# Performance work log

Measured on AMD Instinct MI355X. Metric: run time of the kernel, lower is better.

## Reference

```python
import jax, jax.numpy as jnp
import numpy as np
from jax import lax

K = 4  # scan directions

def setup_inputs() -> dict:
    key = jax.random.key(0)
    ks = jax.random.split(key, 8)
    B, D, H, W = 8, 192, 64, 64
    N, R = 16, 6
    return {
        "x": jax.random.normal(ks[0], (B, D, H, W), jnp.float32),
        "x_proj_weight": jax.random.normal(ks[1], (K, R + 2 * N, D), jnp.float32) * (D ** -0.5),
        "dt_projs_weight": jax.random.normal(ks[2], (K, D, R), jnp.float32) * (R ** -0.5),
        "dt_projs_bias": jax.random.normal(ks[3], (K, D), jnp.float32) * 0.1,
        "A_logs": jax.random.uniform(ks[4], (K * D, N), jnp.float32, 0.0, 1.0),
        "Ds": jnp.ones((K * D,), jnp.float32),
        "out_norm_weight": jnp.ones((D,), jnp.float32),
        "out_norm_bias": jnp.zeros((D,), jnp.float32),
    }


def _ss2d_core(x, x_proj_weight, dt_projs_weight, dt_projs_bias, A_logs, Ds,
               out_norm_weight, out_norm_bias):
    B, D, H, W = x.shape
    L = H * W
    N = A_logs.shape[1]
    R = dt_projs_weight.shape[2]

    # ---- CrossScan: 4 traversal orders of the 2D grid ----
    x_flat = x.reshape(B, D, L)                                   # row-major
    x_t = jnp.transpose(x, (0, 1, 3, 2)).reshape(B, D, L)         # col-major
    xs = jnp.stack([x_flat, x_t, x_flat[..., ::-1], x_t[..., ::-1]], axis=1)  # (B,K,D,L)

    # ---- input-dependent projections ----
    x_dbl = jnp.einsum('bkdl,kcd->bkcl', xs, x_proj_weight)       # (B,K,R+2N,L)
    dts, Bs, Cs = jnp.split(x_dbl, [R, R + N], axis=2)            # (B,K,R,L),(B,K,N,L),(B,K,N,L)
    dts = jnp.einsum('bkrl,kdr->bkdl', dts, dt_projs_weight)      # (B,K,D,L)

    A = -jnp.exp(A_logs.astype(jnp.float32)).reshape(K, D, N)     # (K,D,N)
    delta = jax.nn.softplus(dts + dt_projs_bias[None, :, :, None])  # (B,K,D,L)
    u = xs

    # ---- selective scan over L (sequential state recurrence) ----
    def step(h, inp):
        d_t, u_t, b_t, c_t = inp                                   # (B,K,D),(B,K,D),(B,K,N),(B,K,N)
        dA = jnp.exp(d_t[..., None] * A)                           # (B,K,D,N)
        h = dA * h + (d_t * u_t)[..., None] * b_t[:, :, None, :]
        y = jnp.einsum('bkdn,bkn->bkd', h, c_t)
        return h, y

    h0 = jnp.zeros((B, K, D, N), jnp.float32)
    inputs = (jnp.moveaxis(delta, -1, 0), jnp.moveaxis(u, -1, 0),
              jnp.moveaxis(Bs, -1, 0), jnp.moveaxis(Cs, -1, 0))
    _, ys = lax.scan(step, h0, inputs)                             # (L,B,K,D)
    ys = jnp.moveaxis(ys, 0, -1)                                   # (B,K,D,L)
    ys = ys + u * Ds.reshape(K, D)[None, :, :, None]               # skip term D*u

    # ---- CrossMerge: undo flips/transposes and sum the 4 directions ----
    ys2 = ys[:, 0:2] + ys[:, 2:4][..., ::-1]                        # (B,2,D,L)
    y = ys2[:, 0] + jnp.transpose(ys2[:, 1].reshape(B, D, W, H), (0, 1, 3, 2)).reshape(B, D, L)

    # ---- out_norm: LayerNorm over channel dim, NHWC layout ----
    y = jnp.transpose(y.reshape(B, D, H, W), (0, 2, 3, 1))          # (B,H,W,D)
    mean = jnp.mean(y, axis=-1, keepdims=True)
    var = jnp.var(y, axis=-1, keepdims=True)
    y = (y - mean) * lax.rsqrt(var + 1e-5) * out_norm_weight + out_norm_bias
    return y.astype(x.dtype)


def reference(x, x_proj_weight, dt_projs_weight, dt_projs_bias, A_logs, Ds,
              out_norm_weight, out_norm_bias):
    return _ss2d_core(x, x_proj_weight, dt_projs_weight, dt_projs_bias,
                      A_logs, Ds, out_norm_weight, out_norm_bias)
```

## Files before the change

### kernel.cpp

```cpp
#include <hip/hip_runtime.h>
#include <hip/hip_bf16.h>

#define B_  8
#define D_  192
#define H_  64
#define W_  64
#define L_  4096
#define K_  4
#define N_  16
#define R_  6
#define C_  38
#define CP  40
#define CL_ 64
#define NC_ 64

using bf16 = __hip_bfloat16;
typedef float v2f __attribute__((ext_vector_type(2)));
typedef short v8s __attribute__((ext_vector_type(8)));
typedef float f32x4 __attribute__((ext_vector_type(4)));

static __device__ __forceinline__ float softplus_f(float x) {
    return fmaxf(x, 0.f) + __logf(1.f + __expf(-fabsf(x)));
}
static __device__ __forceinline__ float bflo(unsigned u) {
    return __uint_as_float(u << 16);
}

__global__ __launch_bounds__(256) void k_transpose(const float* __restrict__ x,
                                                   bf16* __restrict__ xp0b,
                                                   bf16* __restrict__ xp1b) {
    __shared__ float tile[32][33];
    int bi = blockIdx.x;
    int pg = bi & 127;
    int dg = (bi >> 7) % 6;
    int b  = bi / (128 * 6);
    int tx = threadIdx.x & 31;
    int ty = threadIdx.x >> 5;
    size_t xbase = (size_t)b * D_ * L_;
    #pragma unroll
    for (int i = 0; i < 4; i++) {
        int d = dg * 32 + ty + i * 8;
        tile[ty + i * 8][tx] = x[xbase + (size_t)d * L_ + pg * 32 + tx];
    }
    __syncthreads();
    #pragma unroll
    for (int i = 0; i < 4; i++) {
        int p = pg * 32 + ty + i * 8;
        float v = tile[tx][ty + i * 8];
        bf16 vb = __float2bfloat16(v);
        int d = dg * 32 + tx;
        xp0b[((size_t)b * L_ + p) * D_ + d] = vb;
        int hh = p >> 6, ww = p & 63;
        int r = ww * 64 + hh;
        xp1b[((size_t)b * L_ + r) * D_ + d] = vb;
    }
}

__global__ __launch_bounds__(256) void k_proj(const bf16* __restrict__ xp0b,
                                              const bf16* __restrict__ xp1b,
                                              const float* __restrict__ Wp,
                                              float* __restrict__ xdbl) {
    __shared__ __align__(16) unsigned short xt[64 * 200];
    __shared__ __align__(16) unsigned short wt[48 * 200];
    int blk  = blockIdx.x;
    int tile = blk & 63;
    int bk   = blk >> 6;
    int k    = bk & 3;
    int b    = bk >> 2;
    const bf16* xpb = (k & 1) ? xp1b : xp0b;
    int g0 = (k < 2) ? tile * 64 : (L_ - 64 - tile * 64);

    unsigned* wtu = (unsigned*)wt;
    for (int i = threadIdx.x; i < 1000; i += 256) wtu[3800 + i] = 0u;
    const float2* wsrc = (const float2*)(Wp + (size_t)k * C_ * D_);
    for (int i = threadIdx.x; i < 3648; i += 256) {
        float2 wv2 = wsrc[i];
        int c = i / 96, dp = i % 96;
        bf16 b0 = __float2bfloat16(wv2.x), b1 = __float2bfloat16(wv2.y);
        unsigned pack = ((unsigned)(*(unsigned short*)&b1) << 16) |
                        (unsigned)(*(unsigned short*)&b0);
        wtu[c * 100 + dp] = pack;
    }
    const uint4* src = (const uint4*)(xpb + ((size_t)b * L_ + g0) * D_);
    for (int i = threadIdx.x; i < 1536; i += 256) {
        uint4 v = src[i];
        int row = i / 24, cg = i % 24;
        int rr = (k < 2) ? row : 63 - row;
        *((uint4*)(xt + rr * 200 + cg * 8)) = v;
    }
    __syncthreads();

    int wv   = threadIdx.x >> 6;
    int lane = threadIdx.x & 63;
    int m0   = wv * 16;
    int mrow = lane & 15;
    int kq   = lane >> 4;

    f32x4 acc[3];
    #pragma unroll
    for (int nt = 0; nt < 3; nt++) acc[nt] = (f32x4){0.f, 0.f, 0.f, 0.f};

    const unsigned short* arow = xt + (m0 + mrow) * 200 + kq * 8;
    const unsigned short* brow = wt + mrow * 200 + kq * 8;
    #pragma unroll
    for (int kt = 0; kt < 6; kt++) {
        v8s af = *(const v8s*)(arow + kt * 32);
        #pragma unroll
        for (int nt = 0; nt < 3; nt++) {
            v8s bf = *(const v8s*)(brow + nt * 16 * 200 + kt * 32);
            acc[nt] = __builtin_amdgcn_mfma_f32_16x16x32_bf16(af, bf, acc[nt], 0, 0, 0);
        }
    }

    int l0g = tile * 64;
    #pragma unroll
    for (int nt = 0; nt < 3; nt++) {
        int c = nt * 16 + mrow;
        if (c < C_) {
            #pragma unroll
            for (int r = 0; r < 4; r++) {
                int m = m0 + kq * 4 + r;
                xdbl[((size_t)bk * L_ + l0g + m) * CP + c] = acc[nt][r];
            }
        }
    }
}

__global__ __launch_bounds__(192) void k_scanA(const float* __restrict__ xdbl,
                                               const bf16* __restrict__ xp0b,
                                               const bf16* __restrict__ xp1b,
                                               const float* __restrict__ dtw,
                                               const float* __restrict__ dtb,
                                               const float* __restrict__ Alog,
                                               const float* __restrict__ Dsk,
                                               bf16* __restrict__ Pst,
                                               bf16* __restrict__ Hloc,
                                               bf16* __restrict__ ys) {
    __shared__ __align__(16) unsigned short ut[CL_ * D_];
    int blk = blockIdx.x;
    int c   = blk & (NC_ - 1);
    int bk  = blk >> 6;
    int k   = bk & 3;
    int b   = bk >> 2;
    int d   = threadIdx.x;

    int l0 = c * CL_;
    const bf16* xpb = (k & 1) ? xp1b : xp0b;
    int base_lu = (k < 2) ? l0 : (L_ - CL_ - l0);
    {
        const uint4* usrc = (const uint4*)(xpb + ((size_t)b * L_ + base_lu) * D_);
        uint4* udst = (uint4*)ut;
        #pragma unroll
        for (int i = 0; i < 8; i++) udst[threadIdx.x + i * 192] = usrc[threadIdx.x + i * 192];
    }

    v2f A2[8];
    #pragma unroll
    for (int i = 0; i < 8; i++) {
        A2[i].x = -__expf(Alog[((size_t)(k * D_ + d)) * N_ + 2*i])   * 1.44269504f;
        A2[i].y = -__expf(Alog[((size_t)(k * D_ + d)) * N_ + 2*i+1]) * 1.44269504f;
    }
    float wr[R_];
    #pragma unroll
    for (int r = 0; r < R_; r++) wr[r] = dtw[(k * D_ + d) * R_ + r];
    float bias = dtb[k * D_ + d];
    float DsV  = Dsk[k * D_ + d];

    v2f h[8];
    #pragma unroll
    for (int i = 0; i < 8; i++) { h[i].x = 0.f; h[i].y = 0.f; }
    float S = 0.f;
    const float* rb = xdbl + ((size_t)bk * L_ + l0) * CP;
    bf16* yp  = ys   + ((size_t)bk * L_ + l0) * D_ + d;

    int uidx  = ((k < 2) ? 0 : (CL_ - 1)) * D_ + d;
    int ustep = (k < 2) ? D_ : -D_;
    __syncthreads();

    #pragma unroll 2
    for (int s = 0; s < CL_; s++) {
        const float4* r4 = (const float4*)(rb + s * CP);
        float4 q0 = r4[0], q1 = r4[1], q2 = r4[2], q3 = r4[3], q4 = r4[4];
        float4 q5 = r4[5], q6 = r4[6], q7 = r4[7], q8 = r4[8], q9 = r4[9];
        float dpre = bias + wr[0]*q0.x + wr[1]*q0.y + wr[2]*q0.z + wr[3]*q0.w
                          + wr[4]*q1.x + wr[5]*q1.y;
        float delta = softplus_f(dpre);
        float u = bflo(ut[uidx]);  uidx += ustep;
        float du = delta * u;
        S += delta;
        v2f Bv[8] = {{q1.z,q1.w},{q2.x,q2.y},{q2.z,q2.w},{q3.x,q3.y},
                     {q3.z,q3.w},{q4.x,q4.y},{q4.z,q4.w},{q5.x,q5.y}};
        v2f Cv[8] = {{q5.z,q5.w},{q6.x,q6.y},{q6.z,q6.w},{q7.x,q7.y},
                     {q7.z,q7.w},{q8.x,q8.y},{q8.z,q8.w},{q9.x,q9.y}};
        v2f y2; y2.x = 0.f; y2.y = 0.f;
        #pragma unroll
        for (int i = 0; i < 8; i++) {
            v2f t = A2[i] * delta;
            v2f dA;
            dA.x = __builtin_amdgcn_exp2f(t.x);
            dA.y = __builtin_amdgcn_exp2f(t.y);
            h[i] = dA * h[i] + Bv[i] * du;
            y2   = y2 + h[i] * Cv[i];
        }
        float y = y2.x + y2.y;
        *yp = __float2bfloat16(y + u * DsV);
        yp += D_;
    }
    size_t o = ((size_t)blk * D_ + d) * N_;
    #pragma unroll
    for (int i = 0; i < 8; i++) {
        v2f t = A2[i] * S;
        Pst[o + 2*i]   = __float2bfloat16(__builtin_amdgcn_exp2f(t.x));
        Pst[o + 2*i+1] = __float2bfloat16(__builtin_amdgcn_exp2f(t.y));
        Hloc[o + 2*i]   = __float2bfloat16(h[i].x);
        Hloc[o + 2*i+1] = __float2bfloat16(h[i].y);
    }
}

__global__ __launch_bounds__(256) void k_pass2(const bf16* __restrict__ Pst,
                                               const bf16* __restrict__ Hloc,
                                               bf16* __restrict__ Hin) {
    int idx = blockIdx.x * 256 + threadIdx.x;
    int bk  = idx / (D_ * N_);
    int dn  = idx % (D_ * N_);
    float hh = 0.f;
    for (int c = 0; c < NC_; c++) {
        size_t o = ((size_t)bk * NC_ + c) * (D_ * N_) + dn;
        Hin[o] = __float2bfloat16(hh);
        hh = __bfloat162float(Pst[o]) * hh + __bfloat162float(Hloc[o]);
    }
}

__global__ __launch_bounds__(192) void k_corr(const float* __restrict__ xdbl,
                                              const float* __restrict__ dtw,
                                              const float* __restrict__ dtb,
                                              const float* __restrict__ Alog,
                                              const bf16* __restrict__ Hin,
                                              bf16* __restrict__ ys) {
    int blk = blockIdx.x;
    int c   = blk & (NC_ - 1);
    if (c == 0) return;
    int bk  = blk >> 6;
    int k   = bk & 3;
    int d   = threadIdx.x;

    float A2[N_];
    float aMax = -1e30f;
    #pragma unroll
    for (int n = 0; n < N_; n++) {
        A2[n] = -__expf(Alog[((size_t)(k * D_ + d)) * N_ + n]) * 1.44269504f;
        aMax = fmaxf(aMax, A2[n]);
    }
    float wr[R_];
    #pragma unroll
    for (int r = 0; r < R_; r++) wr[r] = dtw[(k * D_ + d) * R_ + r];
    float bias = dtb[k * D_ + d];

    float g[N_];
    size_t o = ((size_t)blk * D_ + d) * N_;
    #pragma unroll
    for (int n = 0; n < N_; n++) g[n] = __bfloat162float(Hin[o + n]);

    int l0 = c * CL_;
    const float* rb = xdbl + ((size_t)bk * L_ + l0) * CP;
    bf16* yp = ys + ((size_t)bk * L_ + l0) * D_ + d;

    float S = 0.f;
    for (int s = 0; s < CL_; s++) {
        const float4* r4 = (const float4*)(rb + s * CP);
        float4 q0 = r4[0], q1 = r4[1];
        float dpre = bias + wr[0]*q0.x + wr[1]*q0.y + wr[2]*q0.z + wr[3]*q0.w
                          + wr[4]*q1.x + wr[5]*q1.y;
        S += softplus_f(dpre);
        bool alive = (aMax * S > -18.f);
        if (__ballot(alive) == 0ull) break;
        const float4* c4 = (const float4*)(rb + s * CP + 20);
        float4 c5 = c4[0], c6 = c4[1], c7 = c4[2], c8 = c4[3], c9 = c4[4];
        float Cv[N_] = {c5.z,c5.w,c6.x,c6.y,c6.z,c6.w,c7.x,c7.y,
                        c7.z,c7.w,c8.x,c8.y,c8.z,c8.w,c9.x,c9.y};
        float acc = 0.f;
        #pragma unroll
        for (int n = 0; n < N_; n++) {
            float e = __builtin_amdgcn_exp2f(A2[n] * S);
            acc = fmaf(Cv[n], e * g[n], acc);
        }
        float y = __bfloat162float(*yp) + acc;
        *yp = __float2bfloat16(y);
        yp += D_;
    }
}

__global__ __launch_bounds__(192) void k_merge_ln(const bf16* __restrict__ ys,
                                                  const float* __restrict__ gw,
                                                  const float* __restrict__ gb,
                                                  float* __restrict__ out) {
    int p = blockIdx.x & (L_ - 1);
    int b = blockIdx.x >> 12;
    int d = threadIdx.x;
    int hh = p >> 6, ww = p & 63;
    int l1 = ww * 64 + hh;
    size_t base = (size_t)b * K_ * L_ * D_;
    float v = __bfloat162float(ys[base + ((size_t)0 * L_ + p) * D_ + d])
            + __bfloat162float(ys[base + ((size_t)2 * L_ + (L_ - 1 - p)) * D_ + d])
            + __bfloat162float(ys[base + ((size_t)1 * L_ + l1) * D_ + d])
            + __bfloat162float(ys[base + ((size_t)3 * L_ + (L_ - 1 - l1)) * D_ + d]);
    float s1 = v, s2 = v * v;
    #pragma unroll
    for (int off = 32; off; off >>= 1) {
        s1 += __shfl_down(s1, off);
        s2 += __shfl_down(s2, off);
    }
    __shared__ float aS[3], aQ[3];
    int wid = d >> 6, lane = d & 63;
    if (lane == 0) { aS[wid] = s1; aQ[wid] = s2; }
    __syncthreads();
    float ts1 = aS[0] + aS[1] + aS[2];
    float ts2 = aQ[0] + aQ[1] + aQ[2];
    float mean = ts1 * (1.f / 192.f);
    float var  = ts2 * (1.f / 192.f) - mean * mean;
    float inv  = rsqrtf(var + 1e-5f);
    out[((size_t)b * L_ + p) * D_ + d] = (v - mean) * inv * gw[d] + gb[d];
}

extern "C" void kernel_launch(void* const* d_in, const int* in_sizes, int n_in,
                              void* d_out, int out_size, void* d_ws, size_t ws_size,
                              hipStream_t stream) {
    const float* x    = (const float*)d_in[0];
    const float* Wp   = (const float*)d_in[1];
    const float* dtw  = (const float*)d_in[2];
    const float* dtb  = (const float*)d_in[3];
    const float* Alog = (const float*)d_in[4];
    const float* Dsk  = (const float*)d_in[5];
    const float* gw   = (const float*)d_in[6];
    const float* gb   = (const float*)d_in[7];
    float* out = (float*)d_out;

    char* ws = (char*)d_ws;
    const size_t S1b = (size_t)B_ * L_ * D_ * 2;
    const size_t Sx  = (size_t)B_ * K_ * L_ * CP * 4;
    const size_t Ss  = (size_t)B_ * K_ * NC_ * D_ * N_ * 2;
    char* p = ws;
    bf16*  xp0b = (bf16*)p;   p += S1b;
    bf16*  xp1b = (bf16*)p;   p += S1b;
    float* xdbl = (float*)p;  p += Sx;
    bf16*  Pst  = (bf16*)p;   p += Ss;
    bf16*  Hloc = (bf16*)p;   p += Ss;
    bf16*  Hin  = (bf16*)p;   p += Ss;
    bf16*  ys   = (bf16*)p;

    k_transpose<<<B_ * 6 * 128, 256, 0, stream>>>(x, xp0b, xp1b);
    k_proj<<<B_ * K_ * (L_ / 64), 256, 0, stream>>>(xp0b, xp1b, Wp, xdbl);
    k_scanA<<<B_ * K_ * NC_, 192, 0, stream>>>(xdbl, xp0b, xp1b, dtw, dtb, Alog, Dsk,
                                               Pst, Hloc, ys);
    k_pass2<<<(B_ * K_ * D_ * N_) / 256, 256, 0, stream>>>(Pst, Hloc, Hin);
    k_corr<<<B_ * K_ * NC_, 192, 0, stream>>>(xdbl, dtw, dtb, Alog, Hin, ys);
    k_merge_ln<<<B_ * L_, 192, 0, stream>>>(ys, gw, gb, out);
}
```

Measured before the change: 263.7 us.

## Stage xdbl rows in LDS and software-pipeline row and u loads in scans

Measured after the change: 277.8 us. 1.05x slower.

```diff
diff --git a/kernel.cpp b/kernel.cpp
--- a/kernel.cpp
+++ b/kernel.cpp
@@ -126,7 +126,53 @@
     }
 }
 
-__global__ __launch_bounds__(192) void k_scanA(const float* __restrict__ xdbl,
+struct Q10 { float4 q0, q1, q2, q3, q4, q5, q6, q7, q8, q9; };
+struct Q7  { float4 q0, q1, q5, q6, q7, q8, q9; };
+
+static __device__ __forceinline__ Q10 loadq10(const float4* base, int row) {
+    const float4* r = base + row * 10;
+    Q10 t;
+    t.q0 = r[0]; t.q1 = r[1]; t.q2 = r[2]; t.q3 = r[3]; t.q4 = r[4];
+    t.q5 = r[5]; t.q6 = r[6]; t.q7 = r[7]; t.q8 = r[8]; t.q9 = r[9];
+    return t;
+}
+static __device__ __forceinline__ Q7 loadq7(const float4* base, int row) {
+    const float4* r = base + row * 10;
+    Q7 t;
+    t.q0 = r[0]; t.q1 = r[1];
+    t.q5 = r[5]; t.q6 = r[6]; t.q7 = r[7]; t.q8 = r[8]; t.q9 = r[9];
+    return t;
+}
+
+static __device__ __forceinline__ void scan_step(const Q10& P, float u,
+                                                 const v2f* A2, const float* wr,
+                                                 float bias, float DsV,
+                                                 v2f* h, float& S, bf16*& yp) {
+    float dpre = bias + wr[0]*P.q0.x + wr[1]*P.q0.y + wr[2]*P.q0.z + wr[3]*P.q0.w
+                      + wr[4]*P.q1.x + wr[5]*P.q1.y;
+    float delta = softplus_f(dpre);
+    float du = delta * u;
+    S += delta;
+    v2f Bv[8] = {{P.q1.z,P.q1.w},{P.q2.x,P.q2.y},{P.q2.z,P.q2.w},{P.q3.x,P.q3.y},
+                 {P.q3.z,P.q3.w},{P.q4.x,P.q4.y},{P.q4.z,P.q4.w},{P.q5.x,P.q5.y}};
+    v2f Cv[8] = {{P.q5.z,P.q5.w},{P.q6.x,P.q6.y},{P.q6.z,P.q6.w},{P.q7.x,P.q7.y},
+                 {P.q7.z,P.q7.w},{P.q8.x,P.q8.y},{P.q8.z,P.q8.w},{P.q9.x,P.q9.y}};
+    v2f y2; y2.x = 0.f; y2.y = 0.f;
+    #pragma unroll
+    for (int i = 0; i < 8; i++) {
+        v2f t = A2[i] * delta;
+        v2f dA;
+        dA.x = __builtin_amdgcn_exp2f(t.x);
+        dA.y = __builtin_amdgcn_exp2f(t.y);
+        h[i] = dA * h[i] + Bv[i] * du;
+        y2   = y2 + h[i] * Cv[i];
+    }
+    float yv = y2.x + y2.y;
+    *yp = __float2bfloat16(yv + u * DsV);
+    yp += D_;
+}
+
+__global__ __launch_bounds__(192, 3) void k_scanA(const float* __restrict__ xdbl,
                                                const bf16* __restrict__ xp0b,
                                                const bf16* __restrict__ xp1b,
                                                const float* __restrict__ dtw,
@@ -136,7 +182,7 @@
                                                bf16* __restrict__ Pst,
                                                bf16* __restrict__ Hloc,
                                                bf16* __restrict__ ys) {
-    __shared__ __align__(16) unsigned short ut[CL_ * D_];
+    __shared__ __align__(16) float qs[CL_ * CP];
     int blk = blockIdx.x;
     int c   = blk & (NC_ - 1);
     int bk  = blk >> 6;
@@ -146,12 +192,17 @@
 
     int l0 = c * CL_;
     const bf16* xpb = (k & 1) ? xp1b : xp0b;
-    int base_lu = (k < 2) ? l0 : (L_ - CL_ - l0);
+    int l_start = (k < 2) ? l0 : (L_ - 1 - l0);
+    intptr_t sD = (k < 2) ? (intptr_t)D_ : -(intptr_t)D_;
+    const unsigned short* ub =
+        (const unsigned short*)xpb + ((size_t)b * L_ + l_start) * D_ + d;
+
     {
-        const uint4* usrc = (const uint4*)(xpb + ((size_t)b * L_ + base_lu) * D_);
-        uint4* udst = (uint4*)ut;
+        const uint4* src4 = (const uint4*)(xdbl + ((size_t)bk * L_ + l0) * CP);
+        uint4* dst4 = (uint4*)qs;
         #pragma unroll
-        for (int i = 0; i < 8; i++) udst[threadIdx.x + i * 192] = usrc[threadIdx.x + i * 192];
+        for (int i = 0; i < 3; i++) dst4[threadIdx.x + i * 192] = src4[threadIdx.x + i * 192];
+        if (threadIdx.x < 64) dst4[threadIdx.x + 576] = src4[threadIdx.x + 576];
     }
 
     v2f A2[8];
@@ -170,42 +221,30 @@
     #pragma unroll
     for (int i = 0; i < 8; i++) { h[i].x = 0.f; h[i].y = 0.f; }
     float S = 0.f;
-    const float* rb = xdbl + ((size_t)bk * L_ + l0) * CP;
     bf16* yp  = ys   + ((size_t)bk * L_ + l0) * D_ + d;
 
-    int uidx  = ((k < 2) ? 0 : (CL_ - 1)) * D_ + d;
-    int ustep = (k < 2) ? D_ : -D_;
+    unsigned short u_a = ub[0];
+    unsigned short u_b = ub[sD];
+    const unsigned short* upf = ub + 2 * sD;
+
     __syncthreads();
-
-    #pragma unroll 2
-    for (int s = 0; s < CL_; s++) {
-        const float4* r4 = (const float4*)(rb + s * CP);
-        float4 q0 = r4[0], q1 = r4[1], q2 = r4[2], q3 = r4[3], q4 = r4[4];
-        float4 q5 = r4[5], q6 = r4[6], q7 = r4[7], q8 = r4[8], q9 = r4[9];
-        float dpre = bias + wr[0]*q0.x + wr[1]*q0.y + wr[2]*q0.z + wr[3]*q0.w
-                          + wr[4]*q1.x + wr[5]*q1.y;
-        float delta = softplus_f(dpre);
-        float u = bflo(ut[uidx]);  uidx += ustep;
-        float du = delta * u;
-        S += delta;
-        v2f Bv[8] = {{q1.z,q1.w},{q2.x,q2.y},{q2.z,q2.w},{q3.x,q3.y},
-                     {q3.z,q3.w},{q4.x,q4.y},{q4.z,q4.w},{q5.x,q5.y}};
-        v2f Cv[8] = {{q5.z,q5.w},{q6.x,q6.y},{q6.z,q6.w},{q7.x,q7.y},
-                     {q7.z,q7.w},{q8.x,q8.y},{q8.z,q8.w},{q9.x,q9.y}};
-        v2f y2; y2.x = 0.f; y2.y = 0.f;
-        #pragma unroll
-        for (int i = 0; i < 8; i++) {
-            v2f t = A2[i] * delta;
-            v2f dA;
-            dA.x = __builtin_amdgcn_exp2f(t.x);
-            dA.y = __builtin_amdgcn_exp2f(t.y);
-            h[i] = dA * h[i] + Bv[i] * du;
-            y2   = y2 + h[i] * Cv[i];
-        }
-        float y = y2.x + y2.y;
-        *yp = __float2bfloat16(y + u * DsV);
-        yp += D_;
-    }
+    const float4* q4 = (const float4*)qs;
+
+    Q10 qa = loadq10(q4, 0);
+    for (int s = 0; s < CL_ - 2; s += 2) {
+        Q10 qb = loadq10(q4, s + 1);
+        { unsigned short uu = u_a; u_a = *upf; upf += sD;
+          scan_step(qa, bflo((unsigned)uu), A2, wr, bias, DsV, h, S, yp); }
+        qa = loadq10(q4, s + 2);
+        { unsigned short uu = u_b; u_b = *upf; upf += sD;
+          scan_step(qb, bflo((unsigned)uu), A2, wr, bias, DsV, h, S, yp); }
+    }
+    {
+        Q10 qb = loadq10(q4, CL_ - 1);
+        scan_step(qa, bflo((unsigned)u_a), A2, wr, bias, DsV, h, S, yp);
+        scan_step(qb, bflo((unsigned)u_b), A2, wr, bias, DsV, h, S, yp);
+    }
+
     size_t o = ((size_t)blk * D_ + d) * N_;
     #pragma unroll
     for (int i = 0; i < 8; i++) {
@@ -231,12 +270,36 @@
     }
 }
 
-__global__ __launch_bounds__(192) void k_corr(const float* __restrict__ xdbl,
+static __device__ __forceinline__ bool corr_step(const Q7& P,
+                                                 const float* A2, const float* g,
+                                                 const float* wr, float bias,
+                                                 float aMax, float& S, bf16*& yp) {
+    float dpre = bias + wr[0]*P.q0.x + wr[1]*P.q0.y + wr[2]*P.q0.z + wr[3]*P.q0.w
+                      + wr[4]*P.q1.x + wr[5]*P.q1.y;
+    S += softplus_f(dpre);
+    bool alive = (aMax * S > -18.f);
+    if (__ballot(alive) == 0ull) return false;
+    float Cv[N_] = {P.q5.z,P.q5.w,P.q6.x,P.q6.y,P.q6.z,P.q6.w,P.q7.x,P.q7.y,
+                    P.q7.z,P.q7.w,P.q8.x,P.q8.y,P.q8.z,P.q8.w,P.q9.x,P.q9.y};
+    float acc = 0.f;
+    #pragma unroll
+    for (int n = 0; n < N_; n++) {
+        float e = __builtin_amdgcn_exp2f(A2[n] * S);
+        acc = fmaf(Cv[n], e * g[n], acc);
+    }
+    float y = __bfloat162float(*yp) + acc;
+    *yp = __float2bfloat16(y);
+    yp += D_;
+    return true;
+}
+
+__global__ __launch_bounds__(192, 3) void k_corr(const float* __restrict__ xdbl,
                                               const float* __restrict__ dtw,
                                               const float* __restrict__ dtb,
                                               const float* __restrict__ Alog,
                                               const bf16* __restrict__ Hin,
                                               bf16* __restrict__ ys) {
+    __shared__ __align__(16) float qs[CL_ * CP];
     int blk = blockIdx.x;
     int c   = blk & (NC_ - 1);
     if (c == 0) return;
@@ -244,6 +307,15 @@
     int k   = bk & 3;
     int d   = threadIdx.x;
 
+    int l0 = c * CL_;
+    {
+        const uint4* src4 = (const uint4*)(xdbl + ((size_t)bk * L_ + l0) * CP);
+        uint4* dst4 = (uint4*)qs;
+        #pragma unroll
+        for (int i = 0; i < 3; i++) dst4[threadIdx.x + i * 192] = src4[threadIdx.x + i * 192];
+        if (threadIdx.x < 64) dst4[threadIdx.x + 576] = src4[threadIdx.x + 576];
+    }
+
     float A2[N_];
     float aMax = -1e30f;
     #pragma unroll
@@ -261,32 +333,25 @@
     #pragma unroll
     for (int n = 0; n < N_; n++) g[n] = __bfloat162float(Hin[o + n]);
 
-    int l0 = c * CL_;
-    const float* rb = xdbl + ((size_t)bk * L_ + l0) * CP;
     bf16* yp = ys + ((size_t)bk * L_ + l0) * D_ + d;
-
+    __syncthreads();
+    const float4* q4 = (const float4*)qs;
     float S = 0.f;
-    for (int s = 0; s < CL_; s++) {
-        const float4* r4 = (const float4*)(rb + s * CP);
-        float4 q0 = r4[0], q1 = r4[1];
-        float dpre = bias + wr[0]*q0.x + wr[1]*q0.y + wr[2]*q0.z + wr[3]*q0.w
-                          + wr[4]*q1.x + wr[5]*q1.y;
-        S += softplus_f(dpre);
-        bool alive = (aMax * S > -18.f);
-        if (__ballot(alive) == 0ull) break;
-        const float4* c4 = (const float4*)(rb + s * CP + 20);
-        float4 c5 = c4[0], c6 = c4[1], c7 = c4[2], c8 = c4[3], c9 = c4[4];
-        float Cv[N_] = {c5.z,c5.w,c6.x,c6.y,c6.z,c6.w,c7.x,c7.y,
-                        c7.z,c7.w,c8.x,c8.y,c8.z,c8.w,c9.x,c9.y};
-        float acc = 0.f;
-        #pragma unroll
-        for (int n = 0; n < N_; n++) {
-            float e = __builtin_amdgcn_exp2f(A2[n] * S);
-            acc = fmaf(Cv[n], e * g[n], acc);
+
+    Q7 qa = loadq7(q4, 0);
+    bool go = true;
+    for (int s = 0; s < CL_ - 2 && go; s += 2) {
+        Q7 qb = loadq7(q4, s + 1);
+        go = corr_step(qa, A2, g, wr, bias, aMax, S, yp);
+        if (go) {
+            qa = loadq7(q4, s + 2);
+            go = corr_step(qb, A2, g, wr, bias, aMax, S, yp);
         }
-        float y = __bfloat162float(*yp) + acc;
-        *yp = __float2bfloat16(y);
-        yp += D_;
+    }
+    if (go) {
+        Q7 qb = loadq7(q4, CL_ - 1);
+        if (corr_step(qa, A2, g, wr, bias, aMax, S, yp))
+            corr_step(qb, A2, g, wr, bias, aMax, S, yp);
     }
 }
 
```
